# Kernel optimization log

Hardware: AMD Instinct MI355X
Metric: run time of the kernel (lower is better)

Reference implementation:

```python
import jax, jax.numpy as jnp
import numpy as np

B, SQ, SK, D, UNITS = 4, 2048, 2048, 1024, 1024

def setup_inputs() -> dict:
    key = jax.random.key(0)
    ks = jax.random.split(key, 5)
    scale = 1.0 / np.sqrt(D)
    return {
        "q": jax.random.normal(ks[0], (B, SQ, D), dtype=jnp.float32),
        "k": jax.random.normal(ks[1], (B, SK, D), dtype=jnp.float32),
        "v": jax.random.normal(ks[2], (B, SK, D), dtype=jnp.float32),
        "W1_w": jax.random.normal(ks[3], (D, UNITS), dtype=jnp.float32) * scale,
        "W1_b": jnp.zeros((UNITS,), dtype=jnp.float32),
        "W2_w": jax.random.normal(ks[4], (D, UNITS), dtype=jnp.float32) * scale,
        "W2_b": jnp.zeros((UNITS,), dtype=jnp.float32),
    }

def reference(q, k, v, W1_w, W1_b, W2_w, W2_b):
    # Dense projections (keras Dense: x @ W + b)
    l1 = q @ W1_w + W1_b            # [B, Sq, units]
    l2 = k @ W2_w + W2_b            # [B, Sk, units]
    # score = l1 @ l2^T, scaled by sqrt(score.shape[2]) == sqrt(Sk) (as in original)
    inv_scale = 1.0 / np.sqrt(k.shape[1]).astype(np.float32)
    score = jnp.einsum('bqu,bku->bqk', l1, l2) * inv_scale  # [B, Sq, Sk]
    dist = jax.nn.softmax(score, axis=-1)
    att = jnp.einsum('bqk,bkd->bqd', dist, v)               # [B, Sq, d_v]
    return att
```

## Files before the change

### kernel.cpp

```cpp
#include <hip/hip_runtime.h>
#include <cmath>
#include <stdint.h>


typedef short short8 __attribute__((ext_vector_type(8)));
typedef float f32x4 __attribute__((ext_vector_type(4)));
typedef __bf16 bf16x8 __attribute__((ext_vector_type(8)));
typedef unsigned int u32x4 __attribute__((ext_vector_type(4)));

typedef __attribute__((address_space(3))) void lds_void;
typedef __attribute__((address_space(1))) void gbl_void;

__device__ __forceinline__ unsigned short f2b(float x) {
    unsigned u = __builtin_bit_cast(unsigned, x);
    u += 0x7fffu + ((u >> 16) & 1u);
    return (unsigned short)(u >> 16);
}

__global__ void prep_kernel(const float* __restrict__ v,
                            const float* __restrict__ W1,
                            const float* __restrict__ W2,
                            unsigned short* __restrict__ vT,
                            unsigned short* __restrict__ W1t,
                            unsigned short* __restrict__ W2t,
                            float* __restrict__ rs) {
    const int bz = blockIdx.z;
    const int t = threadIdx.x;
    const int tid2 = blockIdx.y * 64 + blockIdx.x;

    if (bz == 4 && tid2 >= 256 && tid2 < 288) {
        if (rs) rs[(tid2 - 256) * 256 + t] = 0.f;
        return;
    }

    __shared__ float tile[64][65];
    const float* in;
    unsigned short* out;
    int R, C;
    if (bz < 4) {
        R = 2048; C = 1024;
        in = v + (long)bz * R * C;
        out = vT + (long)bz * R * C;
    } else {
        R = 1024; C = 1024;
        if (tid2 >= 256) return;
        in = (bz == 4) ? W1 : W2;
        out = (bz == 4) ? W1t : W2t;
    }
    const int rt = (tid2 >> 4) * 64;
    const int ct = (tid2 & 15) * 64;

    {
        const int rr = t >> 2;
        const int cb = (t & 3) * 16;
        const float* src = in + (long)(rt + rr) * C + ct + cb;
#pragma unroll
        for (int u = 0; u < 4; u++) {
            float4 a = *(const float4*)(src + 4 * u);
            tile[rr][cb + 4 * u + 0] = a.x;
            tile[rr][cb + 4 * u + 1] = a.y;
            tile[rr][cb + 4 * u + 2] = a.z;
            tile[rr][cb + 4 * u + 3] = a.w;
        }
    }
    __syncthreads();
    {
        const int cc = t >> 2;
        const int rb = (t & 3) * 16;
        unsigned short* dst = out + (long)(ct + cc) * R + rt + rb;
#pragma unroll
        for (int u = 0; u < 2; u++) {
            union { short8 v8; unsigned short us[8]; } o;
#pragma unroll
            for (int e = 0; e < 8; e++) o.us[e] = f2b(tile[rb + 8 * u + e][cc]);
            *(short8*)(dst + 8 * u) = o.v8;
        }
    }
}

__device__ __forceinline__ void load16_to_lds(const unsigned short* g,
                                              unsigned short* l) {
    __builtin_amdgcn_global_load_lds((gbl_void*)g, (lds_void*)l, 16, 0, 0);
}

template <int MODE, int CASTA>
__global__ __launch_bounds__(512, 4) void gemm256_kernel(
                               const unsigned short* __restrict__ A,
                               const unsigned short* __restrict__ Bt,
                               const float* __restrict__ bias0,
                               const float* __restrict__ bias1,
                               float* __restrict__ rowsum,
                               void* __restrict__ Cout,
                               int M, int N, int K,
                               float scale,
                               long sA, long sB, long sC,
                               const float* __restrict__ Afq,
                               const float* __restrict__ Afk) {
    __shared__ __align__(16) unsigned short As[256 * 64];
    __shared__ __align__(16) unsigned short Bs[128 * 64];

    int bx, by, bz;
    {
        const int nx = gridDim.x;
        const int Rt = gridDim.y * gridDim.z;
        if ((Rt & 7) == 0) {
            int flat = ((int)blockIdx.z * gridDim.y + blockIdx.y) * nx + blockIdx.x;
            int rpx = Rt >> 3;
            int c = flat & 7;
            int j = flat >> 3;
            bx = j / rpx;
            int yg = c * rpx + (j - bx * rpx);
            bz = yg / gridDim.y;
            by = yg - bz * gridDim.y;
        } else {
            bx = blockIdx.x; by = blockIdx.y; bz = blockIdx.z;
        }
    }

    Bt += (long)bz * sB;

    const int t = threadIdx.x;
    const int lane = t & 63;
    const int wave = t >> 6;
    const int wm = wave >> 1, wn = wave & 1;
    const int row0 = by * 256;
    const int col0 = bx * 128;

    const int rS = lane >> 3;
    const int kOffS = ((lane & 7) ^ rS) * 8;
    const unsigned short* gA[4];
    const float* fA[4];
    unsigned short* lA[4];
    const unsigned short* gB[2];
    unsigned short* lB[2];
#pragma unroll
    for (int i = 0; i < 4; i++) {
        const int rowl = wave * 32 + i * 8;
        lA[i] = As + rowl * 64;
        if (CASTA) {
            const float* Af = bz ? Afk : Afq;
            fA[i] = Af + (long)(row0 + rowl + rS) * K + kOffS;
        } else {
            gA[i] = A + (long)bz * sA + (long)(row0 + rowl + rS) * K + kOffS;
        }
    }
#pragma unroll
    for (int i = 0; i < 2; i++) {
        const int rowl = wave * 16 + i * 8;
        gB[i] = Bt + (long)(col0 + rowl + rS) * K + kOffS;
        lB[i] = Bs + rowl * 64;
    }

    const int lr = lane & 15;
    const int quad = lane >> 4;
    const int pc0 = (quad ^ (lr & 7)) * 8;
    const int pc1 = ((4 + quad) ^ (lr & 7)) * 8;

    f32x4 acc[4][4];
#pragma unroll
    for (int i = 0; i < 4; i++)
#pragma unroll
        for (int j = 0; j < 4; j++) acc[i][j] = f32x4{0.f, 0.f, 0.f, 0.f};

    for (int k0 = 0; k0 < K; k0 += 64) {
#pragma unroll
        for (int i = 0; i < 2; i++) load16_to_lds(gB[i] + k0, lB[i]);
        if (CASTA) {
#pragma unroll
            for (int i = 0; i < 4; i++) {
                const float* s = fA[i] + k0;
                float4 x = *(const float4*)(s);
                float4 y = *(const float4*)(s + 4);
                unsigned w0, w1, w2, w3;
                asm("v_cvt_pk_bf16_f32 %0, %1, %2" : "=v"(w0) : "v"(x.x), "v"(x.y));
                asm("v_cvt_pk_bf16_f32 %0, %1, %2" : "=v"(w1) : "v"(x.z), "v"(x.w));
                asm("v_cvt_pk_bf16_f32 %0, %1, %2" : "=v"(w2) : "v"(y.x), "v"(y.y));
                asm("v_cvt_pk_bf16_f32 %0, %1, %2" : "=v"(w3) : "v"(y.z), "v"(y.w));
                *(u32x4*)(lA[i] + lane * 8) = u32x4{w0, w1, w2, w3};
            }
        } else {
#pragma unroll
            for (int i = 0; i < 4; i++) load16_to_lds(gA[i] + k0, lA[i]);
        }
        __syncthreads();

#pragma unroll
        for (int ks = 0; ks < 2; ks++) {
            const int pc = ks ? pc1 : pc0;
            bf16x8 a[4], b[4];
#pragma unroll
            for (int i = 0; i < 4; i++) {
                a[i] = __builtin_bit_cast(bf16x8,
                    *(const short8*)(As + (wm * 64 + i * 16 + lr) * 64 + pc));
                b[i] = __builtin_bit_cast(bf16x8,
                    *(const short8*)(Bs + (wn * 64 + i * 16 + lr) * 64 + pc));
            }
#pragma unroll
            for (int i = 0; i < 4; i++)
#pragma unroll
                for (int j = 0; j < 4; j++)
                    acc[i][j] = __builtin_amdgcn_mfma_f32_16x16x32_bf16(
                        a[i], b[j], acc[i][j], 0, 0, 0);
        }
        __syncthreads();
    }

    const long cbase = (long)bz * sC;

    if (MODE == 0) {
        const float* bp = (bz && bias1) ? bias1 : bias0;
#pragma unroll
        for (int j = 0; j < 4; j++) {
            const int gcol = col0 + wn * 64 + j * 16 + lr;
            const float bv = bp[gcol];
#pragma unroll
            for (int i = 0; i < 4; i++) {
                const int growb = row0 + wm * 64 + i * 16 + quad * 4;
#pragma unroll
                for (int r = 0; r < 4; r++) {
                    float val = acc[i][j][r] * scale + bv;
                    ((unsigned short*)Cout)[cbase + (long)(growb + r) * N + gcol] = f2b(val);
                }
            }
        }
    } else {
        float psum[4][4];
#pragma unroll
        for (int i = 0; i < 4; i++)
#pragma unroll
            for (int r = 0; r < 4; r++) psum[i][r] = 0.f;
#pragma unroll
        for (int j = 0; j < 4; j++) {
            const int gcol = col0 + wn * 64 + j * 16 + lr;
#pragma unroll
            for (int i = 0; i < 4; i++) {
                const int growb = row0 + wm * 64 + i * 16 + quad * 4;
#pragma unroll
                for (int r = 0; r < 4; r++) {
                    float e = __expf(acc[i][j][r] * scale);
                    psum[i][r] += e;
                    ((unsigned short*)Cout)[cbase + (long)(growb + r) * N + gcol] = f2b(e);
                }
            }
        }
#pragma unroll
        for (int i = 0; i < 4; i++)
#pragma unroll
            for (int r = 0; r < 4; r++) {
                float s = psum[i][r];
                s += __shfl_xor(s, 1);
                s += __shfl_xor(s, 2);
                s += __shfl_xor(s, 4);
                s += __shfl_xor(s, 8);
                if (lr == 0) {
                    const int grow = row0 + wm * 64 + i * 16 + quad * 4 + r;
                    atomicAdd(rowsum + (long)bz * M + grow, s);
                }
            }
    }
}

__global__ __launch_bounds__(512, 4) void att512_kernel(
        const unsigned short* __restrict__ A,
        const unsigned short* __restrict__ Bt,
        const float* __restrict__ rowsum,
        float* __restrict__ out) {
    __shared__ __align__(16) unsigned short As[128 * 64];
    __shared__ __align__(16) unsigned short Bs[128 * 64];

    int bx, by, bz;
    {
        const int nx = gridDim.x;
        const int Rt = gridDim.y * gridDim.z;
        int flat = ((int)blockIdx.z * gridDim.y + blockIdx.y) * nx + blockIdx.x;
        int rpx = Rt >> 3;
        int c = flat & 7;
        int j = flat >> 3;
        bx = j / rpx;
        int yg = c * rpx + (j - bx * rpx);
        bz = yg / gridDim.y;
        by = yg - bz * gridDim.y;
    }

    const int M = 2048, N = 1024, K = 2048;
    const long sA = (long)M * K, sB = (long)N * K, sC = (long)M * N;
    const unsigned short* Ab  = A  + (long)bz * sA;
    const unsigned short* Btb = Bt + (long)bz * sB;

    const int t = threadIdx.x;
    const int lane = t & 63;
    const int w = t >> 6;
    const int wm = w >> 1, wn = w & 1;
    const int row0 = by * 128;
    const int col0 = bx * 128;

    const int rS = lane >> 3;
    const int kOffS = ((lane & 7) ^ rS) * 8;
    const unsigned short* gA[2];
    unsigned short* lA[2];
    const unsigned short* gB[2];
    unsigned short* lB[2];
#pragma unroll
    for (int i = 0; i < 2; i++) {
        const int rowl = w * 16 + i * 8;
        gA[i] = Ab  + (long)(row0 + rowl + rS) * K + kOffS;
        lA[i] = As + rowl * 64;
        gB[i] = Btb + (long)(col0 + rowl + rS) * K + kOffS;
        lB[i] = Bs + rowl * 64;
    }

    const int lr = lane & 15;
    const int quad = lane >> 4;
    const int pc0 = (quad ^ (lr & 7)) * 8;
    const int pc1 = ((4 + quad) ^ (lr & 7)) * 8;

    f32x4 acc[2][4];
#pragma unroll
    for (int i = 0; i < 2; i++)
#pragma unroll
        for (int j = 0; j < 4; j++) acc[i][j] = f32x4{0.f, 0.f, 0.f, 0.f};

    for (int k0 = 0; k0 < K; k0 += 64) {
#pragma unroll
        for (int i = 0; i < 2; i++) {
            load16_to_lds(gA[i] + k0, lA[i]);
            load16_to_lds(gB[i] + k0, lB[i]);
        }
        __syncthreads();
#pragma unroll
        for (int ks = 0; ks < 2; ks++) {
            const int pc = ks ? pc1 : pc0;
            bf16x8 a[2], b[4];
#pragma unroll
            for (int i = 0; i < 2; i++)
                a[i] = __builtin_bit_cast(bf16x8,
                    *(const short8*)(As + (wm * 32 + i * 16 + lr) * 64 + pc));
#pragma unroll
            for (int j = 0; j < 4; j++)
                b[j] = __builtin_bit_cast(bf16x8,
                    *(const short8*)(Bs + (wn * 64 + j * 16 + lr) * 64 + pc));
#pragma unroll
            for (int i = 0; i < 2; i++)
#pragma unroll
                for (int j = 0; j < 4; j++)
                    acc[i][j] = __builtin_amdgcn_mfma_f32_16x16x32_bf16(
                        a[i], b[j], acc[i][j], 0, 0, 0);
        }
        __syncthreads();
    }

    const long cbase = (long)bz * sC;
#pragma unroll
    for (int i = 0; i < 2; i++) {
        const int growb = row0 + wm * 32 + i * 16 + quad * 4;
#pragma unroll
        for (int r = 0; r < 4; r++) {
            const float inv = 1.0f / rowsum[(long)bz * M + growb + r];
#pragma unroll
            for (int j = 0; j < 4; j++) {
                const int gcol = col0 + wn * 64 + j * 16 + lr;
                out[cbase + (long)(growb + r) * N + gcol] = acc[i][j][r] * inv;
            }
        }
    }
}

extern "C" void kernel_launch(void* const* d_in, const int* in_sizes, int n_in,
                              void* d_out, int out_size, void* d_ws, size_t ws_size,
                              hipStream_t stream) {
    const float* q   = (const float*)d_in[0];
    const float* k   = (const float*)d_in[1];
    const float* v   = (const float*)d_in[2];
    const float* W1w = (const float*)d_in[3];
    const float* W1b = (const float*)d_in[4];
    const float* W2w = (const float*)d_in[5];
    const float* W2b = (const float*)d_in[6];
    float* out = (float*)d_out;

    const int B = 4, SQ = 2048, SK = 2048, D = 1024, U = 1024;
    char* ws = (char*)d_ws;
    const size_t MB = 1024 * 1024;
    unsigned short* vT  = (unsigned short*)(ws + 32 * MB);
    unsigned short* W1t = (unsigned short*)(ws + 48 * MB);
    unsigned short* W2t = (unsigned short*)(ws + 50 * MB);
    unsigned short* l1  = (unsigned short*)(ws + 52 * MB);
    unsigned short* l2  = (unsigned short*)(ws + 68 * MB);
    unsigned short* sc  = (unsigned short*)(ws + 0);

    float* rowsum;
    bool prep_zeroes_rowsum;
    if (ws_size >= 85 * MB) {
        rowsum = (float*)(ws + 84 * MB);
        prep_zeroes_rowsum = true;
    } else {
        rowsum = (float*)(ws + 50 * MB);
        prep_zeroes_rowsum = false;
    }

    prep_kernel<<<dim3(64, 8, 6), 256, 0, stream>>>(
        v, W1w, W2w, vT, W1t, W2t,
        prep_zeroes_rowsum ? rowsum : nullptr);
    gemm256_kernel<0, 1><<<dim3(U / 128, (B * SQ) / 256, 2), 512, 0, stream>>>(
        nullptr, W1t, W1b, W2b, nullptr, l1, B * SQ, U, D, 1.0f,
        0, (long)1024 * 1024, (long)8 * 1024 * 1024, q, k);
    if (!prep_zeroes_rowsum)
        hipMemsetAsync(rowsum, 0, (size_t)B * SQ * sizeof(float), stream);
    const float invs = 1.0f / sqrtf((float)SK);
    gemm256_kernel<1, 0><<<dim3(SK / 128, SQ / 256, B), 512, 0, stream>>>(
        l1, l2, nullptr, nullptr, rowsum, sc, SQ, SK, U, invs,
        (long)SQ * U, (long)SK * U, (long)SQ * SK, nullptr, nullptr);
    att512_kernel<<<dim3(D / 128, SQ / 128, B), 512, 0, stream>>>(
        sc, vT, rowsum, out);
}
```

Before: 267.7 us.

## Stream fp32 activations to LDS asynchronously and convert to bf16 at fragment load

Replaces the projection GEMM's register-staged fp32 load and bf16 convert with a dedicated kernel. It copies fp32 A tiles straight into swizzled LDS via global_load_lds and converts to bf16 when reading MFMA fragments. The aim is to remove the blocking global-to-register load from each k-iteration so loads overlap like the bf16 path. The trade-off is doubled A tile LDS footprint (limits occupancy) and the conversion being repeated by each wave column that reads the tile.

```diff
diff --git a/kernel.cpp b/kernel.cpp
--- a/kernel.cpp
+++ b/kernel.cpp
@@ -83,19 +83,143 @@
     __builtin_amdgcn_global_load_lds((gbl_void*)g, (lds_void*)l, 16, 0, 0);
 }
 
-template <int MODE, int CASTA>
+__global__ __launch_bounds__(512, 4) void l1l2f_kernel(
+        const float* __restrict__ Afq,
+        const float* __restrict__ Afk,
+        const unsigned short* __restrict__ Btw,
+        const float* __restrict__ b1,
+        const float* __restrict__ b2,
+        unsigned short* __restrict__ Cout) {
+    const int M = 8192, N = 1024, K = 1024;
+    __shared__ __align__(16) float Asf[256 * 64];
+    __shared__ __align__(16) unsigned short Bs[128 * 64];
+
+    int bx, by, bz;
+    {
+        const int nx = gridDim.x;
+        const int Rt = gridDim.y * gridDim.z;
+        int flat = ((int)blockIdx.z * gridDim.y + blockIdx.y) * nx + blockIdx.x;
+        int rpx = Rt >> 3;
+        int c = flat & 7;
+        int j = flat >> 3;
+        bx = j / rpx;
+        int yg = c * rpx + (j - bx * rpx);
+        bz = yg / gridDim.y;
+        by = yg - bz * gridDim.y;
+    }
+
+    const float* Af = bz ? Afk : Afq;
+    const unsigned short* Bt = Btw + (long)bz * (1024 * 1024);
+
+    const int t = threadIdx.x;
+    const int lane = t & 63;
+    const int wave = t >> 6;
+    const int wm = wave >> 1, wn = wave & 1;
+    const int row0 = by * 256;
+    const int col0 = bx * 128;
+
+    const int srow4 = lane >> 4;
+    const float* fsrc[8];
+#pragma unroll
+    for (int i = 0; i < 8; i++) {
+        const int rw = wave * 32 + i * 4 + srow4;
+        const int ch = (lane & 15) ^ ((i * 4 + srow4) & 15);
+        fsrc[i] = Af + (long)(row0 + rw) * K + ch * 4;
+    }
+
+    const int rS = lane >> 3;
+    const int kOffS = ((lane & 7) ^ rS) * 8;
+    const unsigned short* gB[2];
+    unsigned short* lB[2];
+#pragma unroll
+    for (int i = 0; i < 2; i++) {
+        const int rowl = wave * 16 + i * 8;
+        gB[i] = Bt + (long)(col0 + rowl + rS) * K + kOffS;
+        lB[i] = Bs + rowl * 64;
+    }
+
+    const int lr = lane & 15;
+    const int quad = lane >> 4;
+    const int pcB0 = (quad ^ (lr & 7)) * 8;
+    const int pcB1 = ((4 + quad) ^ (lr & 7)) * 8;
+
+    f32x4 acc[4][4];
+#pragma unroll
+    for (int i = 0; i < 4; i++)
+#pragma unroll
+        for (int j = 0; j < 4; j++) acc[i][j] = f32x4{0.f, 0.f, 0.f, 0.f};
+
+    for (int k0 = 0; k0 < K; k0 += 64) {
+#pragma unroll
+        for (int i = 0; i < 2; i++) load16_to_lds(gB[i] + k0, lB[i]);
+#pragma unroll
+        for (int i = 0; i < 8; i++) {
+            __builtin_amdgcn_global_load_lds(
+                (gbl_void*)(fsrc[i] + k0),
+                (lds_void*)(Asf + (wave * 32 + i * 4) * 64), 16, 0, 0);
+        }
+        __syncthreads();
+
+#pragma unroll
+        for (int ks = 0; ks < 2; ks++) {
+            const int c0 = ks * 8 + quad * 2;
+            const int p0 = (c0 ^ lr) * 4;
+            const int p1 = ((c0 + 1) ^ lr) * 4;
+            bf16x8 a[4], b[4];
+#pragma unroll
+            for (int i = 0; i < 4; i++) {
+                const float* base = Asf + (wm * 64 + i * 16 + lr) * 64;
+                float4 lo = *(const float4*)(base + p0);
+                float4 hi = *(const float4*)(base + p1);
+                unsigned w0, w1, w2, w3;
+                asm("v_cvt_pk_bf16_f32 %0, %1, %2" : "=v"(w0) : "v"(lo.x), "v"(lo.y));
+                asm("v_cvt_pk_bf16_f32 %0, %1, %2" : "=v"(w1) : "v"(lo.z), "v"(lo.w));
+                asm("v_cvt_pk_bf16_f32 %0, %1, %2" : "=v"(w2) : "v"(hi.x), "v"(hi.y));
+                asm("v_cvt_pk_bf16_f32 %0, %1, %2" : "=v"(w3) : "v"(hi.z), "v"(hi.w));
+                a[i] = __builtin_bit_cast(bf16x8, u32x4{w0, w1, w2, w3});
+            }
+            const int pc = ks ? pcB1 : pcB0;
+#pragma unroll
+            for (int j = 0; j < 4; j++)
+                b[j] = __builtin_bit_cast(bf16x8,
+                    *(const short8*)(Bs + (wn * 64 + j * 16 + lr) * 64 + pc));
+#pragma unroll
+            for (int i = 0; i < 4; i++)
+#pragma unroll
+                for (int j = 0; j < 4; j++)
+                    acc[i][j] = __builtin_amdgcn_mfma_f32_16x16x32_bf16(
+                        a[i], b[j], acc[i][j], 0, 0, 0);
+        }
+        __syncthreads();
+    }
+
+    const long cbase = (long)bz * (long)M * N;
+    const float* bp = bz ? b2 : b1;
+#pragma unroll
+    for (int j = 0; j < 4; j++) {
+        const int gcol = col0 + wn * 64 + j * 16 + lr;
+        const float bv = bp[gcol];
+#pragma unroll
+        for (int i = 0; i < 4; i++) {
+            const int growb = row0 + wm * 64 + i * 16 + quad * 4;
+#pragma unroll
+            for (int r = 0; r < 4; r++) {
+                float val = acc[i][j][r] + bv;
+                Cout[cbase + (long)(growb + r) * N + gcol] = f2b(val);
+            }
+        }
+    }
+}
+
+template <int MODE>
 __global__ __launch_bounds__(512, 4) void gemm256_kernel(
                                const unsigned short* __restrict__ A,
                                const unsigned short* __restrict__ Bt,
-                               const float* __restrict__ bias0,
-                               const float* __restrict__ bias1,
                                float* __restrict__ rowsum,
                                void* __restrict__ Cout,
                                int M, int N, int K,
                                float scale,
-                               long sA, long sB, long sC,
-                               const float* __restrict__ Afq,
-                               const float* __restrict__ Afk) {
+                               long sA, long sB, long sC) {
     __shared__ __align__(16) unsigned short As[256 * 64];
     __shared__ __align__(16) unsigned short Bs[128 * 64];
 
@@ -117,6 +241,7 @@
         }
     }
 
+    A  += (long)bz * sA;
     Bt += (long)bz * sB;
 
     const int t = threadIdx.x;
@@ -129,20 +254,14 @@
     const int rS = lane >> 3;
     const int kOffS = ((lane & 7) ^ rS) * 8;
     const unsigned short* gA[4];
-    const float* fA[4];
     unsigned short* lA[4];
     const unsigned short* gB[2];
     unsigned short* lB[2];
 #pragma unroll
     for (int i = 0; i < 4; i++) {
         const int rowl = wave * 32 + i * 8;
+        gA[i] = A + (long)(row0 + rowl + rS) * K + kOffS;
         lA[i] = As + rowl * 64;
-        if (CASTA) {
-            const float* Af = bz ? Afk : Afq;
-            fA[i] = Af + (long)(row0 + rowl + rS) * K + kOffS;
-        } else {
-            gA[i] = A + (long)bz * sA + (long)(row0 + rowl + rS) * K + kOffS;
-        }
     }
 #pragma unroll
     for (int i = 0; i < 2; i++) {
@@ -164,24 +283,9 @@
 
     for (int k0 = 0; k0 < K; k0 += 64) {
 #pragma unroll
+        for (int i = 0; i < 4; i++) load16_to_lds(gA[i] + k0, lA[i]);
+#pragma unroll
         for (int i = 0; i < 2; i++) load16_to_lds(gB[i] + k0, lB[i]);
-        if (CASTA) {
-#pragma unroll
-            for (int i = 0; i < 4; i++) {
-                const float* s = fA[i] + k0;
-                float4 x = *(const float4*)(s);
-                float4 y = *(const float4*)(s + 4);
-                unsigned w0, w1, w2, w3;
-                asm("v_cvt_pk_bf16_f32 %0, %1, %2" : "=v"(w0) : "v"(x.x), "v"(x.y));
-                asm("v_cvt_pk_bf16_f32 %0, %1, %2" : "=v"(w1) : "v"(x.z), "v"(x.w));
-                asm("v_cvt_pk_bf16_f32 %0, %1, %2" : "=v"(w2) : "v"(y.x), "v"(y.y));
-                asm("v_cvt_pk_bf16_f32 %0, %1, %2" : "=v"(w3) : "v"(y.z), "v"(y.w));
-                *(u32x4*)(lA[i] + lane * 8) = u32x4{w0, w1, w2, w3};
-            }
-        } else {
-#pragma unroll
-            for (int i = 0; i < 4; i++) load16_to_lds(gA[i] + k0, lA[i]);
-        }
         __syncthreads();
 
 #pragma unroll
@@ -207,23 +311,7 @@
 
     const long cbase = (long)bz * sC;
 
-    if (MODE == 0) {
-        const float* bp = (bz && bias1) ? bias1 : bias0;
-#pragma unroll
-        for (int j = 0; j < 4; j++) {
-            const int gcol = col0 + wn * 64 + j * 16 + lr;
-            const float bv = bp[gcol];
-#pragma unroll
-            for (int i = 0; i < 4; i++) {
-                const int growb = row0 + wm * 64 + i * 16 + quad * 4;
-#pragma unroll
-                for (int r = 0; r < 4; r++) {
-                    float val = acc[i][j][r] * scale + bv;
-                    ((unsigned short*)Cout)[cbase + (long)(growb + r) * N + gcol] = f2b(val);
-                }
-            }
-        }
-    } else {
+    if (MODE == 1) {
         float psum[4][4];
 #pragma unroll
         for (int i = 0; i < 4; i++)
@@ -400,15 +488,14 @@
     prep_kernel<<<dim3(64, 8, 6), 256, 0, stream>>>(
         v, W1w, W2w, vT, W1t, W2t,
         prep_zeroes_rowsum ? rowsum : nullptr);
-    gemm256_kernel<0, 1><<<dim3(U / 128, (B * SQ) / 256, 2), 512, 0, stream>>>(
-        nullptr, W1t, W1b, W2b, nullptr, l1, B * SQ, U, D, 1.0f,
-        0, (long)1024 * 1024, (long)8 * 1024 * 1024, q, k);
+    l1l2f_kernel<<<dim3(U / 128, (B * SQ) / 256, 2), 512, 0, stream>>>(
+        q, k, W1t, W1b, W2b, l1);
     if (!prep_zeroes_rowsum)
         hipMemsetAsync(rowsum, 0, (size_t)B * SQ * sizeof(float), stream);
     const float invs = 1.0f / sqrtf((float)SK);
-    gemm256_kernel<1, 0><<<dim3(SK / 128, SQ / 256, B), 512, 0, stream>>>(
-        l1, l2, nullptr, nullptr, rowsum, sc, SQ, SK, U, invs,
-        (long)SQ * U, (long)SK * U, (long)SQ * SK, nullptr, nullptr);
+    gemm256_kernel<1><<<dim3(SK / 128, SQ / 256, B), 512, 0, stream>>>(
+        l1, l2, rowsum, sc, SQ, SK, U, invs,
+        (long)SQ * U, (long)SK * U, (long)SQ * SK);
     att512_kernel<<<dim3(D / 128, SQ / 128, B), 512, 0, stream>>>(
         sc, vT, rowsum, out);
 }
```

After: 262.8 us. No clear change (-1.8%).
